# Kernel optimization log

Hardware: AMD Instinct MI355X
Metric: run time of the kernel (lower is better)

Reference implementation:

```python
import jax, jax.numpy as jnp
import numpy as np

N_NODES = 100000
N_EDGES = 1600000
IN_CH = 128
DIM = 128
OUT_CH = 10
NUM_GRAPHS = 128
BN_EPS = 1e-5


def _bn_train(h, gamma, beta):
    # BatchNorm1d in training mode: batch statistics over the node axis
    mean = jnp.mean(h, axis=0)
    var = jnp.var(h, axis=0)
    return (h - mean) * jax.lax.rsqrt(var + BN_EPS) * gamma + beta


def _gin_conv(x, src, dst, W1, b1, gamma, beta, W2, b2):
    # GINConv with eps=0: nn(x + sum_{j in N(i)} x_j)
    agg = jax.ops.segment_sum(x[src], dst, num_segments=x.shape[0])  # [N, d]
    h = (x + agg) @ W1 + b1
    h = jax.nn.relu(_bn_train(h, gamma, beta))
    h = jax.nn.relu(h @ W2 + b2)
    return h


def setup_inputs() -> dict:
    key = jax.random.key(0)
    ks = jax.random.split(key, 16)
    s = 0.02
    inp = {
        "x": jax.random.normal(ks[0], (N_NODES, IN_CH), dtype=jnp.float32),
        "edge_index": jax.random.randint(ks[1], (2, N_EDGES), 0, N_NODES, dtype=jnp.int64),
        "batch": jnp.sort(jax.random.randint(ks[2], (N_NODES,), 0, NUM_GRAPHS, dtype=jnp.int64)),
        # conv1 MLP
        "W1a": jax.random.normal(ks[3], (IN_CH, DIM), dtype=jnp.float32) * s,
        "b1a": jnp.zeros((DIM,), jnp.float32),
        "ga": jnp.ones((DIM,), jnp.float32),
        "ba": jnp.zeros((DIM,), jnp.float32),
        "W2a": jax.random.normal(ks[4], (DIM, DIM), dtype=jnp.float32) * s,
        "b2a": jnp.zeros((DIM,), jnp.float32),
        # conv2 MLP
        "W1b": jax.random.normal(ks[5], (DIM, DIM), dtype=jnp.float32) * s,
        "b1b": jnp.zeros((DIM,), jnp.float32),
        "gb": jnp.ones((DIM,), jnp.float32),
        "bb": jnp.zeros((DIM,), jnp.float32),
        "W2b": jax.random.normal(ks[6], (DIM, DIM), dtype=jnp.float32) * s,
        "b2b": jnp.zeros((DIM,), jnp.float32),
        # readout linears
        "Wl1": jax.random.normal(ks[7], (DIM, DIM), dtype=jnp.float32) * s,
        "bl1": jnp.zeros((DIM,), jnp.float32),
        "Wl2": jax.random.normal(ks[8], (DIM, OUT_CH), dtype=jnp.float32) * s,
        "bl2": jnp.zeros((OUT_CH,), jnp.float32),
    }
    return inp


def reference(x, edge_index, batch, W1a, b1a, ga, ba, W2a, b2a,
              W1b, b1b, gb, bb, W2b, b2b, Wl1, bl1, Wl2, bl2):
    src, dst = edge_index[0], edge_index[1]
    h = _gin_conv(x, src, dst, W1a, b1a, ga, ba, W2a, b2a)
    h = _gin_conv(h, src, dst, W1b, b1b, gb, bb, W2b, b2b)
    pooled = jax.ops.segment_sum(h, batch, num_segments=NUM_GRAPHS)  # [G, d]
    out = jax.nn.relu(pooled @ Wl1 + bl1)
    # dropout p=0.5 is identity in deterministic/eval evaluation
    out = out @ Wl2 + bl2
    return out
```

## Files before the change

### kernel.cpp

```cpp
#include <hip/hip_runtime.h>

#define N_NODES    100000
#define N_EDGES    1600000
#define DIM        128
#define OUT_CH     10
#define NUM_GRAPHS 128
#define BN_EPS     1e-5f

#define BSHIFT   8
#define NB2      391
#define CAP2     5120

typedef __attribute__((ext_vector_type(8))) short short8;
typedef __attribute__((ext_vector_type(4))) float floatx4;

__device__ inline float bf2f(unsigned short u) {
    union { unsigned i; float f; } v; v.i = (unsigned)u << 16; return v.f;
}
__device__ inline unsigned short f2bf(float f) {
    union { float f; unsigned i; } v; v.f = f;
    unsigned r = (v.i + 0x7fffu + ((v.i >> 16) & 1u)) >> 16;
    return (unsigned short)r;
}

__device__ inline void async_cp16(const unsigned short* g, unsigned short* l) {
    __builtin_amdgcn_global_load_lds(
        (const __attribute__((address_space(1))) void*)g,
        (__attribute__((address_space(3))) void*)l, 16, 0, 0);
}

__global__ void k_cvt_x(const float* __restrict__ x, unsigned short* __restrict__ xb,
                        int* __restrict__ gcur, float* __restrict__ stats4,
                        float* __restrict__ pooled) {
    int t = threadIdx.x;
    if (blockIdx.x == 0) {
        for (int i = t; i < NB2 + 1; i += 256) gcur[i] = 0;
        for (int i = t; i < 4 * DIM; i += 256) stats4[i] = 0.f;
        for (int i = t; i < NUM_GRAPHS * DIM; i += 256) pooled[i] = 0.f;
    }
    int idx = blockIdx.x * 256 + t;
    float4 v = ((const float4*)x)[idx];
    ushort4 o;
    o.x = f2bf(v.x); o.y = f2bf(v.y); o.z = f2bf(v.z); o.w = f2bf(v.w);
    ((ushort4*)xb)[idx] = o;
}

__global__ void k_prep_w(const float* __restrict__ W0, const float* __restrict__ W1,
                         const float* __restrict__ W2, const float* __restrict__ W3,
                         unsigned short* __restrict__ Wt) {
    const float* Ws[4] = {W0, W1, W2, W3};
    const float* W = Ws[blockIdx.y];
    unsigned short* o = Wt + blockIdx.y * (DIM * DIM);
    int idx = blockIdx.x * 256 + threadIdx.x;
    int n = idx >> 7, k = idx & 127;
    o[idx] = f2bf(W[k * DIM + n]);
}

__global__ __launch_bounds__(256)
void k_bucket(const int* __restrict__ src, const int* __restrict__ dst,
              int* __restrict__ gcur, unsigned* __restrict__ pairs) {
    __shared__ int h[NB2];
    int t = threadIdx.x;
    for (int i = t; i < NB2; i += 256) h[i] = 0;
    __syncthreads();
    int base = blockIdx.x * 4096;
    #pragma unroll
    for (int i = 0; i < 16; ++i) {
        int idx = base + i * 256 + t;
        if (idx < N_EDGES) atomicAdd(&h[dst[idx] >> BSHIFT], 1);
    }
    __syncthreads();
    for (int i = t; i < NB2; i += 256) h[i] = atomicAdd(&gcur[i], h[i]);
    __syncthreads();
    #pragma unroll
    for (int i = 0; i < 16; ++i) {
        int idx = base + i * 256 + t;
        if (idx < N_EDGES) {
            int d = dst[idx];
            int b = d >> BSHIFT;
            int pos = atomicAdd(&h[b], 1);
            if (pos < CAP2)
                pairs[(size_t)b * CAP2 + pos] = ((unsigned)src[idx] << 8) | (unsigned)(d & 255);
        }
    }
}

__global__ void k_bscan(const int* __restrict__ gcur, int* __restrict__ bbase,
                        int* __restrict__ row_ptr) {
    __shared__ int sh[512];
    int t = threadIdx.x;
    int v = (t < NB2) ? min(gcur[t], CAP2) : 0;
    sh[t] = v; __syncthreads();
    for (int off = 1; off < 512; off <<= 1) {
        int tmp = (t >= off) ? sh[t - off] : 0;
        __syncthreads();
        sh[t] += tmp;
        __syncthreads();
    }
    if (t < NB2) bbase[t] = sh[t] - v;
    if (t == NB2 - 1) { bbase[NB2] = sh[t]; row_ptr[N_NODES] = sh[t]; }
}

__global__ __launch_bounds__(256)
void k_csr(const unsigned* __restrict__ pairs, const int* __restrict__ gcur,
           const int* __restrict__ bbase, int* __restrict__ row_ptr,
           int* __restrict__ col) {
    __shared__ int hist[256];
    __shared__ int cur[256];
    int bi = blockIdx.x, t = threadIdx.x;
    hist[t] = 0; __syncthreads();
    int n = min(gcur[bi], CAP2);
    const unsigned* P = pairs + (size_t)bi * CAP2;
    for (int i = t; i < n; i += 256)
        atomicAdd(&hist[P[i] & 255u], 1);
    __syncthreads();
    int self = hist[t];
    cur[t] = self; __syncthreads();
    for (int off = 1; off < 256; off <<= 1) {
        int tmp = (t >= off) ? cur[t - off] : 0;
        __syncthreads();
        cur[t] += tmp;
        __syncthreads();
    }
    int excl = cur[t] - self;
    int base = bbase[bi];
    int node = (bi << 8) + t;
    if (node < N_NODES) row_ptr[node] = base + excl;
    __syncthreads();
    cur[t] = base + excl;
    __syncthreads();
    for (int i = t; i < n; i += 256) {
        unsigned e = P[i];
        int pos = atomicAdd(&cur[e & 255u], 1);
        col[pos] = (int)(e >> 8);
    }
}

__global__ void k_agg(const unsigned short* __restrict__ X,
                      unsigned short* __restrict__ Out,
                      const int* __restrict__ row_ptr, const int* __restrict__ col) {
    int wid = (blockIdx.x * 256 + threadIdx.x) >> 6;
    if (wid >= N_NODES) return;
    int lane = threadIdx.x & 63;
    int half = lane >> 5, m = lane & 31;
    const ushort4* X4 = (const ushort4*)X;

    float a0=0.f,a1=0.f,a2=0.f,a3=0.f;
    float c0=0.f,c1=0.f,c2=0.f,c3=0.f;
    if (half == 0) {
        ushort4 sv = X4[(size_t)wid * 32 + m];
        a0 = bf2f(sv.x); a1 = bf2f(sv.y); a2 = bf2f(sv.z); a3 = bf2f(sv.w);
    }
    int s = row_ptr[wid], e = row_ptr[wid + 1];
    int p = s + half;
    for (; p + 6 < e; p += 8) {
        int n0 = col[p], n1 = col[p + 2], n2 = col[p + 4], n3 = col[p + 6];
        ushort4 v0 = X4[(size_t)n0 * 32 + m];
        ushort4 v1 = X4[(size_t)n1 * 32 + m];
        ushort4 v2 = X4[(size_t)n2 * 32 + m];
        ushort4 v3 = X4[(size_t)n3 * 32 + m];
        a0 += bf2f(v0.x); a1 += bf2f(v0.y); a2 += bf2f(v0.z); a3 += bf2f(v0.w);
        c0 += bf2f(v1.x); c1 += bf2f(v1.y); c2 += bf2f(v1.z); c3 += bf2f(v1.w);
        a0 += bf2f(v2.x); a1 += bf2f(v2.y); a2 += bf2f(v2.z); a3 += bf2f(v2.w);
        c0 += bf2f(v3.x); c1 += bf2f(v3.y); c2 += bf2f(v3.z); c3 += bf2f(v3.w);
    }
    for (; p < e; p += 2) {
        ushort4 v = X4[(size_t)col[p] * 32 + m];
        a0 += bf2f(v.x); a1 += bf2f(v.y); a2 += bf2f(v.z); a3 += bf2f(v.w);
    }
    a0 += c0; a1 += c1; a2 += c2; a3 += c3;
    a0 += __shfl_xor(a0, 32);
    a1 += __shfl_xor(a1, 32);
    a2 += __shfl_xor(a2, 32);
    a3 += __shfl_xor(a3, 32);
    if (half == 0) {
        ushort4 o;
        o.x = f2bf(a0); o.y = f2bf(a1); o.z = f2bf(a2); o.w = f2bf(a3);
        ((ushort4*)Out)[(size_t)wid * 32 + m] = o;
    }
}

template<bool BN_LOAD, bool STATS, bool RELU_ST>
__global__ __launch_bounds__(256)
void k_gemm(const unsigned short* __restrict__ In, unsigned short* __restrict__ Out,
            const unsigned short* __restrict__ Wt, const float* __restrict__ bias,
            const float* __restrict__ ssum_in, const float* __restrict__ ssq_in,
            const float* __restrict__ gamma, const float* __restrict__ beta,
            float* __restrict__ ssum_out, float* __restrict__ ssq_out) {
    __shared__ __align__(16) unsigned short sB[128 * 128];
    __shared__ float ssc[128], ssh[128];
    __shared__ float s_sum[128], s_sq[128];

    int t = threadIdx.x;
    int w = t >> 6, lane = t & 63;
    int r0 = blockIdx.x * 128;
    int m = lane & 15;
    int q = lane >> 4;

    int rowA0 = min(r0 + w * 32 + m,      N_NODES - 1);
    int rowA1 = min(r0 + w * 32 + 16 + m, N_NODES - 1);
    short8 a0[4], a1[4];
    #pragma unroll
    for (int kk = 0; kk < 4; ++kk) {
        a0[kk] = *(const short8*)(In + (size_t)rowA0 * 128 + kk * 32 + q * 8);
        a1[kk] = *(const short8*)(In + (size_t)rowA1 * 128 + kk * 32 + q * 8);
    }

    #pragma unroll
    for (int u = 0; u < 8; ++u) {
        int i = (w * 8 + u) * 64 + lane;
        int n = i >> 4, p = i & 15;
        async_cp16(Wt + n * 128 + ((p ^ (n & 7)) << 3), sB + (size_t)(w * 8 + u) * 512);
    }
    if (BN_LOAD && t < 128) {
        float mn  = ssum_in[t] * (1.0f / N_NODES);
        float var = ssq_in[t] * (1.0f / N_NODES) - mn * mn;
        float inv = rsqrtf(var + BN_EPS);
        float sc  = gamma[t] * inv;
        ssc[t] = sc; ssh[t] = beta[t] - mn * sc;
    }
    if (STATS && t < 128) { s_sum[t] = 0.f; s_sq[t] = 0.f; }
    __syncthreads();

    if (BN_LOAD) {
        #pragma unroll
        for (int kk = 0; kk < 4; ++kk) {
            int base = kk * 32 + q * 8;
            #pragma unroll
            for (int j = 0; j < 8; ++j) {
                float scj = ssc[base + j], shj = ssh[base + j];
                float f0 = fmaxf(bf2f((unsigned short)a0[kk][j]) * scj + shj, 0.f);
                float f1 = fmaxf(bf2f((unsigned short)a1[kk][j]) * scj + shj, 0.f);
                a0[kk][j] = (short)f2bf(f0);
                a1[kk][j] = (short)f2bf(f1);
            }
        }
    }

    int sw = m & 7;
    floatx4 acc[2][8] = {};
    #pragma unroll
    for (int kk = 0; kk < 4; ++kk) {
        int cp = (kk * 4 + q) ^ sw;
        #pragma unroll
        for (int c = 0; c < 8; ++c) {
            int nr = c * 16 + m;
            short8 b = *(const short8*)&sB[nr * 128 + (cp << 3)];
            acc[0][c] = __builtin_amdgcn_mfma_f32_16x16x32_bf16(b, a0[kk], acc[0][c], 0, 0, 0);
            acc[1][c] = __builtin_amdgcn_mfma_f32_16x16x32_bf16(b, a1[kk], acc[1][c], 0, 0, 0);
        }
    }

    #pragma unroll
    for (int c = 0; c < 8; ++c) {
        int ch0 = c * 16 + q * 4;
        float4 bv = *(const float4*)(bias + ch0);
        float sr[4] = {0,0,0,0}, qr[4] = {0,0,0,0};
        #pragma unroll
        for (int h = 0; h < 2; ++h) {
            int node = r0 + w * 32 + h * 16 + m;
            float v0 = acc[h][c][0] + bv.x;
            float v1 = acc[h][c][1] + bv.y;
            float v2 = acc[h][c][2] + bv.z;
            float v3 = acc[h][c][3] + bv.w;
            if (RELU_ST) {
                v0 = fmaxf(v0, 0.f); v1 = fmaxf(v1, 0.f);
                v2 = fmaxf(v2, 0.f); v3 = fmaxf(v3, 0.f);
            }
            if (node < N_NODES) {
                ushort4 o;
                o.x = f2bf(v0); o.y = f2bf(v1); o.z = f2bf(v2); o.w = f2bf(v3);
                *(ushort4*)(Out + (size_t)node * 128 + ch0) = o;
                if (STATS) {
                    sr[0] += v0; sr[1] += v1; sr[2] += v2; sr[3] += v3;
                    qr[0] += v0*v0; qr[1] += v1*v1; qr[2] += v2*v2; qr[3] += v3*v3;
                }
            }
        }
        if (STATS) {
            #pragma unroll
            for (int msk = 1; msk <= 8; msk <<= 1) {
                #pragma unroll
                for (int r = 0; r < 4; ++r) {
                    sr[r] += __shfl_xor(sr[r], msk);
                    qr[r] += __shfl_xor(qr[r], msk);
                }
            }
            if (m == 0) {
                #pragma unroll
                for (int r = 0; r < 4; ++r) {
                    atomicAdd(&s_sum[ch0 + r], sr[r]);
                    atomicAdd(&s_sq [ch0 + r], qr[r]);
                }
            }
        }
    }
    if (STATS) {
        __syncthreads();
        if (t < 128) {
            atomicAdd(&ssum_out[t], s_sum[t]);
            atomicAdd(&ssq_out [t], s_sq[t]);
        }
    }
}

#define POOL_BLOCKS 512
#define POOL_CHUNK  196
__global__ void k_pool(const unsigned short* __restrict__ h, const int* __restrict__ batch,
                       float* __restrict__ pooled) {
    int c  = threadIdx.x;
    int n0 = blockIdx.x * POOL_CHUNK;
    if (n0 >= N_NODES) return;
    int n1 = min(n0 + POOL_CHUNK, N_NODES);
    int g = batch[n0];
    float acc = 0.f;
    for (int i = n0; i < n1; ++i) {
        int gi = batch[i];
        if (gi != g) { atomicAdd(&pooled[g * DIM + c], acc); acc = 0.f; g = gi; }
        acc += bf2f(h[(size_t)i * DIM + c]);
    }
    atomicAdd(&pooled[g * DIM + c], acc);
}

__global__ void k_readout(const float* __restrict__ pooled,
                          const float* __restrict__ Wl1, const float* __restrict__ bl1,
                          const float* __restrict__ Wl2, const float* __restrict__ bl2,
                          float* __restrict__ out) {
    __shared__ float p[128], r[128];
    int g = blockIdx.x, c = threadIdx.x;
    p[c] = pooled[g * DIM + c];
    __syncthreads();
    float s = bl1[c];
    #pragma unroll 8
    for (int k = 0; k < DIM; ++k) s += p[k] * Wl1[k * DIM + c];
    r[c] = fmaxf(s, 0.f);
    __syncthreads();
    if (c < OUT_CH) {
        float s2 = bl2[c];
        #pragma unroll 8
        for (int k = 0; k < DIM; ++k) s2 += r[k] * Wl2[k * OUT_CH + c];
        out[g * OUT_CH + c] = s2;
    }
}

extern "C" void kernel_launch(void* const* d_in, const int* in_sizes, int n_in,
                              void* d_out, int out_size, void* d_ws, size_t ws_size,
                              hipStream_t stream) {
    const float* x   = (const float*)d_in[0];
    const int*   ei  = (const int*)d_in[1];
    const int*   bat = (const int*)d_in[2];
    const float* W1a = (const float*)d_in[3];
    const float* b1a = (const float*)d_in[4];
    const float* ga  = (const float*)d_in[5];
    const float* ba  = (const float*)d_in[6];
    const float* W2a = (const float*)d_in[7];
    const float* b2a = (const float*)d_in[8];
    const float* W1b = (const float*)d_in[9];
    const float* b1b = (const float*)d_in[10];
    const float* gb  = (const float*)d_in[11];
    const float* bbt = (const float*)d_in[12];
    const float* W2b = (const float*)d_in[13];
    const float* b2b = (const float*)d_in[14];
    const float* Wl1 = (const float*)d_in[15];
    const float* bl1 = (const float*)d_in[16];
    const float* Wl2 = (const float*)d_in[17];
    const float* bl2 = (const float*)d_in[18];
    float* out = (float*)d_out;

    const int* src = ei;
    const int* dst = ei + N_EDGES;

    char* w = (char*)d_ws;
    size_t off = 0;
    auto alloc = [&](size_t bytes) -> char* {
        char* p = w + off; off += (bytes + 255) & ~(size_t)255; return p;
    };
    unsigned short* xb   = (unsigned short*)alloc((size_t)N_NODES * DIM * 2);
    unsigned short* nb0  = (unsigned short*)alloc((size_t)N_NODES * DIM * 2);
    unsigned short* nb1  = (unsigned short*)alloc((size_t)N_NODES * DIM * 2);
    unsigned short* Wtb  = (unsigned short*)alloc((size_t)4 * DIM * DIM * 2);
    unsigned* pairs = (unsigned*)alloc((size_t)NB2 * CAP2 * 4);
    int*   row_ptr = (int*)  alloc((size_t)(N_NODES + 1) * 4);
    int*   col     = (int*)  alloc((size_t)N_EDGES * 4);
    int*   gcur    = (int*)  alloc((NB2 + 1) * 4);
    int*   bbase   = (int*)  alloc((NB2 + 1) * 4);
    float* stats4  = (float*)alloc((size_t)4 * DIM * 4);
    float* pooled  = (float*)alloc((size_t)NUM_GRAPHS * DIM * 4);
    float* ssumA = stats4, *ssqA = stats4 + DIM, *ssumB = stats4 + 2*DIM, *ssqB = stats4 + 3*DIM;

    k_cvt_x<<<(N_NODES * DIM / 4) / 256, 256, 0, stream>>>(x, xb, gcur, stats4, pooled);
    k_prep_w<<<dim3(64, 4), 256, 0, stream>>>(W1a, W2a, W1b, W2b, Wtb);
    const unsigned short* Wt1a = Wtb;
    const unsigned short* Wt2a = Wtb + DIM * DIM;
    const unsigned short* Wt1b = Wtb + 2 * DIM * DIM;
    const unsigned short* Wt2b = Wtb + 3 * DIM * DIM;

    k_bucket<<<(N_EDGES + 4095) / 4096, 256, 0, stream>>>(src, dst, gcur, pairs);
    k_bscan<<<1, 512, 0, stream>>>(gcur, bbase, row_ptr);
    k_csr<<<NB2, 256, 0, stream>>>(pairs, gcur, bbase, row_ptr, col);

    int agg_blocks  = (N_NODES * 64) / 256;
    int gemm_blocks = (N_NODES + 127) / 128;

    k_agg<<<agg_blocks, 256, 0, stream>>>(xb, nb0, row_ptr, col);
    k_gemm<false, true, false><<<gemm_blocks, 256, 0, stream>>>(
        nb0, nb1, Wt1a, b1a, nullptr, nullptr, nullptr, nullptr, ssumA, ssqA);
    k_gemm<true, false, true><<<gemm_blocks, 256, 0, stream>>>(
        nb1, nb0, Wt2a, b2a, ssumA, ssqA, ga, ba, nullptr, nullptr);
    k_agg<<<agg_blocks, 256, 0, stream>>>(nb0, nb1, row_ptr, col);
    k_gemm<false, true, false><<<gemm_blocks, 256, 0, stream>>>(
        nb1, nb0, Wt1b, b1b, nullptr, nullptr, nullptr, nullptr, ssumB, ssqB);
    k_gemm<true, false, true><<<gemm_blocks, 256, 0, stream>>>(
        nb0, nb1, Wt2b, b2b, ssumB, ssqB, gb, bbt, nullptr, nullptr);
    k_pool<<<POOL_BLOCKS, 128, 0, stream>>>(nb1, bat, pooled);
    k_readout<<<NUM_GRAPHS, 128, 0, stream>>>(pooled, Wl1, bl1, Wl2, bl2, out);
}
```

Before: 514.2 us.

## Stage bucket and CSR scatters in LDS, share weight tile across two GEMM row tiles

The bucketing kernel now handles 8192 edges per block and computes local offsets with a block scan. It places pairs in LDS in sorted order before writing them out contiguously, so global scatter writes become coalesced. The CSR kernel likewise sorts columns in LDS and writes col in one linear pass. The GEMM uses 512-thread blocks covering two 128-row tiles that share one LDS copy of the weight matrix, halving weight loads per row. The trade-off is more LDS per block (32KB stage in bucket), which may reduce occupancy.

```diff
diff --git a/kernel.cpp b/kernel.cpp
--- a/kernel.cpp
+++ b/kernel.cpp
@@ -10,6 +10,7 @@
 #define BSHIFT   8
 #define NB2      391
 #define CAP2     5120
+#define NTILES   782
 
 typedef __attribute__((ext_vector_type(8))) short short8;
 typedef __attribute__((ext_vector_type(4))) float floatx4;
@@ -59,29 +60,55 @@
 __global__ __launch_bounds__(256)
 void k_bucket(const int* __restrict__ src, const int* __restrict__ dst,
               int* __restrict__ gcur, unsigned* __restrict__ pairs) {
-    __shared__ int h[NB2];
+    __shared__ int cnt[NB2 + 1];
+    __shared__ int lofs[NB2 + 1];
+    __shared__ int gbase[NB2 + 1];
+    __shared__ int scanA[256], scanB[256];
+    __shared__ int stage[8192];
+
     int t = threadIdx.x;
-    for (int i = t; i < NB2; i += 256) h[i] = 0;
-    __syncthreads();
-    int base = blockIdx.x * 4096;
-    #pragma unroll
-    for (int i = 0; i < 16; ++i) {
-        int idx = base + i * 256 + t;
-        if (idx < N_EDGES) atomicAdd(&h[dst[idx] >> BSHIFT], 1);
-    }
-    __syncthreads();
-    for (int i = t; i < NB2; i += 256) h[i] = atomicAdd(&gcur[i], h[i]);
-    __syncthreads();
-    #pragma unroll
-    for (int i = 0; i < 16; ++i) {
-        int idx = base + i * 256 + t;
-        if (idx < N_EDGES) {
-            int d = dst[idx];
-            int b = d >> BSHIFT;
-            int pos = atomicAdd(&h[b], 1);
-            if (pos < CAP2)
-                pairs[(size_t)b * CAP2 + pos] = ((unsigned)src[idx] << 8) | (unsigned)(d & 255);
-        }
+    for (int i = t; i < NB2 + 1; i += 256) cnt[i] = 0;
+    __syncthreads();
+    int base = blockIdx.x * 8192;
+    int n_e = min(8192, N_EDGES - base);
+    for (int i = t; i < n_e; i += 256)
+        atomicAdd(&cnt[dst[base + i] >> BSHIFT], 1);
+    __syncthreads();
+    int vA = cnt[t];
+    int vB = (t < NB2 - 256) ? cnt[256 + t] : 0;
+    scanA[t] = vA; scanB[t] = vB;
+    __syncthreads();
+    for (int off = 1; off < 256; off <<= 1) {
+        int tA = (t >= off) ? scanA[t - off] : 0;
+        int tB = (t >= off) ? scanB[t - off] : 0;
+        __syncthreads();
+        scanA[t] += tA; scanB[t] += tB;
+        __syncthreads();
+    }
+    lofs[t] = scanA[t] - vA;
+    if (t < NB2 - 256) lofs[256 + t] = scanA[255] + scanB[t] - vB;
+    __syncthreads();
+    for (int i = t; i < NB2; i += 256) {
+        gbase[i] = (cnt[i] > 0) ? atomicAdd(&gcur[i], cnt[i]) : 0;
+        cnt[i] = lofs[i];
+    }
+    __syncthreads();
+    for (int i = t; i < n_e; i += 256) {
+        int d = dst[base + i];
+        int b = d >> BSHIFT;
+        int pos = atomicAdd(&cnt[b], 1);
+        stage[pos] = (int)(((unsigned)src[base + i] << 8) | (unsigned)(d & 255));
+    }
+    __syncthreads();
+    int w = t >> 6, lane = t & 63;
+    for (int b = w; b < NB2; b += 4) {
+        int len = cnt[b] - lofs[b];
+        int g0  = gbase[b];
+        int maxlen = CAP2 - g0; if (maxlen < 0) maxlen = 0;
+        if (len > maxlen) len = maxlen;
+        unsigned* dp = pairs + (size_t)b * CAP2 + g0;
+        const int* sp = stage + lofs[b];
+        for (int i = lane; i < len; i += 64) dp[i] = (unsigned)sp[i];
     }
 }
 
@@ -107,6 +134,7 @@
            int* __restrict__ col) {
     __shared__ int hist[256];
     __shared__ int cur[256];
+    __shared__ int stage[CAP2];
     int bi = blockIdx.x, t = threadIdx.x;
     hist[t] = 0; __syncthreads();
     int n = min(gcur[bi], CAP2);
@@ -126,14 +154,15 @@
     int base = bbase[bi];
     int node = (bi << 8) + t;
     if (node < N_NODES) row_ptr[node] = base + excl;
-    __syncthreads();
-    cur[t] = base + excl;
+    cur[t] = excl;
     __syncthreads();
     for (int i = t; i < n; i += 256) {
         unsigned e = P[i];
         int pos = atomicAdd(&cur[e & 255u], 1);
-        col[pos] = (int)(e >> 8);
-    }
+        stage[pos] = (int)(e >> 8);
+    }
+    __syncthreads();
+    for (int i = t; i < n; i += 256) col[base + i] = stage[i];
 }
 
 __global__ void k_agg(const unsigned short* __restrict__ X,
@@ -181,7 +210,7 @@
 }
 
 template<bool BN_LOAD, bool STATS, bool RELU_ST>
-__global__ __launch_bounds__(256)
+__global__ __launch_bounds__(512)
 void k_gemm(const unsigned short* __restrict__ In, unsigned short* __restrict__ Out,
             const unsigned short* __restrict__ Wt, const float* __restrict__ bias,
             const float* __restrict__ ssum_in, const float* __restrict__ ssq_in,
@@ -193,12 +222,14 @@
 
     int t = threadIdx.x;
     int w = t >> 6, lane = t & 63;
-    int r0 = blockIdx.x * 128;
+    int tm = w >> 2, wv = w & 3;
     int m = lane & 15;
     int q = lane >> 4;
-
-    int rowA0 = min(r0 + w * 32 + m,      N_NODES - 1);
-    int rowA1 = min(r0 + w * 32 + 16 + m, N_NODES - 1);
+    int tile = blockIdx.x * 2 + tm;
+    int r0 = tile * 128;
+
+    int rowA0 = min(r0 + wv * 32 + m,      N_NODES - 1);
+    int rowA1 = min(r0 + wv * 32 + 16 + m, N_NODES - 1);
     short8 a0[4], a1[4];
     #pragma unroll
     for (int kk = 0; kk < 4; ++kk) {
@@ -207,10 +238,10 @@
     }
 
     #pragma unroll
-    for (int u = 0; u < 8; ++u) {
-        int i = (w * 8 + u) * 64 + lane;
+    for (int u = 0; u < 4; ++u) {
+        int i = (w * 4 + u) * 64 + lane;
         int n = i >> 4, p = i & 15;
-        async_cp16(Wt + n * 128 + ((p ^ (n & 7)) << 3), sB + (size_t)(w * 8 + u) * 512);
+        async_cp16(Wt + n * 128 + ((p ^ (n & 7)) << 3), sB + (size_t)(w * 4 + u) * 512);
     }
     if (BN_LOAD && t < 128) {
         float mn  = ssum_in[t] * (1.0f / N_NODES);
@@ -258,7 +289,7 @@
         float sr[4] = {0,0,0,0}, qr[4] = {0,0,0,0};
         #pragma unroll
         for (int h = 0; h < 2; ++h) {
-            int node = r0 + w * 32 + h * 16 + m;
+            int node = r0 + wv * 32 + h * 16 + m;
             float v0 = acc[h][c][0] + bv.x;
             float v1 = acc[h][c][1] + bv.y;
             float v2 = acc[h][c][2] + bv.z;
@@ -395,22 +426,22 @@
     const unsigned short* Wt1b = Wtb + 2 * DIM * DIM;
     const unsigned short* Wt2b = Wtb + 3 * DIM * DIM;
 
-    k_bucket<<<(N_EDGES + 4095) / 4096, 256, 0, stream>>>(src, dst, gcur, pairs);
+    k_bucket<<<(N_EDGES + 8191) / 8192, 256, 0, stream>>>(src, dst, gcur, pairs);
     k_bscan<<<1, 512, 0, stream>>>(gcur, bbase, row_ptr);
     k_csr<<<NB2, 256, 0, stream>>>(pairs, gcur, bbase, row_ptr, col);
 
     int agg_blocks  = (N_NODES * 64) / 256;
-    int gemm_blocks = (N_NODES + 127) / 128;
+    int gemm_blocks = NTILES / 2;
 
     k_agg<<<agg_blocks, 256, 0, stream>>>(xb, nb0, row_ptr, col);
-    k_gemm<false, true, false><<<gemm_blocks, 256, 0, stream>>>(
+    k_gemm<false, true, false><<<gemm_blocks, 512, 0, stream>>>(
         nb0, nb1, Wt1a, b1a, nullptr, nullptr, nullptr, nullptr, ssumA, ssqA);
-    k_gemm<true, false, true><<<gemm_blocks, 256, 0, stream>>>(
+    k_gemm<true, false, true><<<gemm_blocks, 512, 0, stream>>>(
         nb1, nb0, Wt2a, b2a, ssumA, ssqA, ga, ba, nullptr, nullptr);
     k_agg<<<agg_blocks, 256, 0, stream>>>(nb0, nb1, row_ptr, col);
-    k_gemm<false, true, false><<<gemm_blocks, 256, 0, stream>>>(
+    k_gemm<false, true, false><<<gemm_blocks, 512, 0, stream>>>(
         nb1, nb0, Wt1b, b1b, nullptr, nullptr, nullptr, nullptr, ssumB, ssqB);
-    k_gemm<true, false, true><<<gemm_blocks, 256, 0, stream>>>(
+    k_gemm<true, false, true><<<gemm_blocks, 512, 0, stream>>>(
         nb0, nb1, Wt2b, b2b, ssumB, ssqB, gb, bbt, nullptr, nullptr);
     k_pool<<<POOL_BLOCKS, 128, 0, stream>>>(nb1, bat, pooled);
     k_readout<<<NUM_GRAPHS, 128, 0, stream>>>(pooled, Wl1, bl1, Wl2, bl2, out);
```

New measurement: 495.9 us. 1.04x faster.
